# Optimization experiments

Hardware: AMD Instinct MI355X
Metric: run time of the kernel (lower is better)

Reference implementation:

```python
import jax, jax.numpy as jnp
import numpy as np

DIM = 512
HEADS = 8
P = 4  # split_size
SCALE = (DIM // HEADS) ** -0.5  # scale uses full dim//heads as in source


def conv1x1(x, w):
    # x: [b,c,h,w], w: [out,in]
    return jnp.einsum('oc,bchw->bohw', w, x)


def to_windows(t, p1, p2, h):
    # 'b (h d) (x p1) (y p2) -> (b x y) h (p1 p2) d'
    b, c, X, Y = t.shape
    d = c // h
    nx, ny = X // p1, Y // p2
    t = t.reshape(b, h, d, nx, p1, ny, p2)
    t = t.transpose(0, 3, 5, 1, 4, 6, 2)  # b nx ny h p1 p2 d
    return t.reshape(b * nx * ny, h, p1 * p2, d)


def from_windows(t, b, nx, ny, h, p1, p2, d):
    # '(b x y) h (p1 p2) d -> b (h d) (x p1) (y p2)'
    t = t.reshape(b, nx, ny, h, p1, p2, d)
    t = t.transpose(0, 3, 6, 1, 4, 2, 5)  # b h d nx p1 ny p2
    return t.reshape(b, h * d, nx * p1, ny * p2)


def setup_inputs() -> dict:
    key = jax.random.key(0)
    ks = jax.random.split(key, 6)
    s = 0.02
    return {
        'fmap': jax.random.normal(ks[0], (8, DIM, 64, 64), jnp.float32),
        'w_qk': jax.random.normal(ks[1], (2 * DIM, DIM), jnp.float32) * s,
        'w_v': jax.random.normal(ks[2], (DIM, DIM), jnp.float32) * s,
        'w_v_vert': jax.random.normal(ks[3], (DIM // 2, DIM // 2), jnp.float32) * s,
        'w_v_horiz': jax.random.normal(ks[4], (DIM // 2, DIM // 2), jnp.float32) * s,
        'w_proj': jax.random.normal(ks[5], (DIM, DIM), jnp.float32) * s,
    }


def reference(fmap, w_qk, w_v, w_v_vert, w_v_horiz, w_proj):
    b, c, X, Y = fmap.shape
    h, half = HEADS, c // 2
    d = half // h  # per-window head dim

    qk = conv1x1(fmap, w_qk)
    q, k = jnp.split(qk, 2, axis=1)
    v = conv1x1(fmap, w_v)

    # horizontal branch: first half channels, windows (X, P)
    qh = to_windows(q[:, :half], X, P, h)
    kh = to_windows(k[:, :half], X, P, h)
    vh = to_windows(v[:, :half], X, P, h)
    lepe_h = vh  # source bug: to_v_horizontal output discarded, raw v used as LePE

    # vertical branch: second half channels, windows (P, Y)
    qv = to_windows(q[:, half:], P, Y, h)
    kv = to_windows(k[:, half:], P, Y, h)
    vv = to_windows(v[:, half:], P, Y, h)
    lepe_v = to_windows(conv1x1(v[:, half:], w_v_vert), P, Y, h)

    def attend(qw, kw, vw, lepe):
        attn = jax.nn.softmax((qw * SCALE) @ jnp.swapaxes(kw, -1, -2), axis=-1)
        return attn @ vw + lepe

    out_h = attend(qh, kh, vh, lepe_h)
    out_v = attend(qv, kv, vv, lepe_v)

    oh = from_windows(out_h, b, X // X, Y // P, h, X, P, d)
    ov = from_windows(out_v, b, X // P, Y // Y, h, P, Y, d)
    out = jnp.concatenate([oh, ov], axis=1)
    return fmap + conv1x1(out, w_proj)
```

## Files before the change

kernel.cpp:

```cpp
#include <hip/hip_runtime.h>
#include <hip/hip_bf16.h>

#define NPIX 4096
#define SCALE_L2E 0.18033688f

typedef unsigned short ushort_t;
typedef __attribute__((ext_vector_type(8))) short bf16x8;
typedef __attribute__((ext_vector_type(4))) float f32x4;
typedef __attribute__((ext_vector_type(8))) unsigned short us8;

__device__ __forceinline__ float bf2f(ushort_t u) {
  union { unsigned int i; float f; } v; v.i = ((unsigned int)u) << 16; return v.f;
}
__device__ __forceinline__ ushort_t f2bf(float f) {
  union { float f; unsigned int i; } v; v.f = f;
  unsigned int r = v.i + 0x7fffu + ((v.i >> 16) & 1u);
  return (ushort_t)(r >> 16);
}
__device__ __forceinline__ unsigned int cvtpk(float lo, float hi) {
  unsigned int r;
  asm volatile("v_cvt_pk_bf16_f32 %0, %1, %2" : "=v"(r) : "v"(lo), "v"(hi));
  return r;
}

__device__ __forceinline__ void gload16(const void* g, void* l) {
  __builtin_amdgcn_global_load_lds(
      (const __attribute__((address_space(1))) void*)g,
      (__attribute__((address_space(3))) void*)l, 16, 0, 0);
}

#define VMW(N) asm volatile("s_waitcnt vmcnt(" #N ")" ::: "memory")
#define BARRS do { __builtin_amdgcn_s_barrier(); \
                   __builtin_amdgcn_sched_barrier(0); } while (0)

__global__ __launch_bounds__(256) void prep_w(const float* __restrict__ wqk,
                                              const float* __restrict__ wv,
                                              const float* __restrict__ wproj,
                                              ushort_t* __restrict__ WQKV,
                                              ushort_t* __restrict__ WPb) {
  const int i = (blockIdx.x * 256 + threadIdx.x) * 4;
  const int seg = i >> 18, off = i & 262143;
  const float* src;
  ushort_t* dst;
  float sc = 1.0f;
  if (seg == 0)      { src = wqk;          dst = WQKV;               sc = SCALE_L2E; }
  else if (seg == 1) { src = wqk + 262144; dst = WQKV + 262144; }
  else if (seg == 2) { src = wv;           dst = WQKV + 2 * 262144; }
  else               { src = wproj;        dst = WPb; }
  const float4 v = *(const float4*)&src[off];
  ushort4 o = make_ushort4(f2bf(v.x * sc), f2bf(v.y * sc),
                           f2bf(v.z * sc), f2bf(v.w * sc));
  *(ushort4*)&dst[off] = o;
}

__global__ __launch_bounds__(256) void lepe_w(const float* __restrict__ wvv,
                                              const float* __restrict__ wv,
                                              ushort_t* __restrict__ out) {
  const int i = blockIdx.x, tid = threadIdx.x;
  float a0 = 0.f, a1 = 0.f;
  for (int c = 0; c < 256; ++c) {
    const float wc = wvv[i * 256 + c];
    a0 = fmaf(wc, wv[(size_t)(256 + c) * 512 + tid], a0);
    a1 = fmaf(wc, wv[(size_t)(256 + c) * 512 + 256 + tid], a1);
  }
  out[(size_t)i * 512 + tid] = f2bf(a0);
  out[(size_t)i * 512 + 256 + tid] = f2bf(a1);
}

__global__ __launch_bounds__(256) void transpose_cast(const float* __restrict__ fmap,
                                                      ushort_t* __restrict__ XT) {
  const int b = blockIdx.z, p0 = blockIdx.x * 64, c0 = blockIdx.y * 64;
  const int tid = threadIdx.x;
  __shared__ float t[64][65];
  const float* src = fmap + ((size_t)b * 512 + c0) * NPIX + p0;
  const int pr = tid & 63;
  #pragma unroll
  for (int i = 0; i < 16; ++i) {
    const int cr = i * 4 + (tid >> 6);
    t[cr][pr] = src[(size_t)cr * NPIX + pr];
  }
  __syncthreads();
  const int pw = tid >> 2, cwb = (tid & 3) * 16;
  us8 o0, o1;
  #pragma unroll
  for (int i = 0; i < 8; ++i) o0[i] = f2bf(t[cwb + i][pw]);
  #pragma unroll
  for (int i = 0; i < 8; ++i) o1[i] = f2bf(t[cwb + 8 + i][pw]);
  ushort_t* dst = XT + ((size_t)b * NPIX + p0 + pw) * 512 + c0 + cwb;
  *(us8*)&dst[0] = o0;
  *(us8*)&dst[8] = o1;
}

__global__ __launch_bounds__(256) void gemm128(
    const ushort_t* __restrict__ A, const ushort_t* __restrict__ B,
    ushort_t* __restrict__ qkT, ushort_t* __restrict__ vbuf,
    float* __restrict__ outF, const float* __restrict__ Res, int mode)
{
  const int b = blockIdx.z;
  const int p0 = blockIdx.x * 128;
  const int o0 = blockIdx.y * 128;
  const int tid = threadIdx.x;
  const int lane = tid & 63, w = tid >> 6;
  const int wrow = (w >> 1) * 64, wcol = (w & 1) * 64;
  const int g = lane >> 4, q16 = lane & 15;

  __shared__ __attribute__((aligned(16))) ushort_t lds[3 * 8192];

  const ushort_t* Bb = B + (size_t)b * NPIX * 512;

  f32x4 acc[4][4];
  #pragma unroll
  for (int m = 0; m < 4; ++m)
    #pragma unroll
    for (int n = 0; n < 4; ++n) acc[m][n] = (f32x4){0.f, 0.f, 0.f, 0.f};

  auto Ap = [&](int buf) { return lds + buf * 8192; };
  auto Bp = [&](int buf) { return lds + buf * 8192 + 4096; };

  auto stage = [&](int buf, int kb) {
    #pragma unroll
    for (int i = 0; i < 2; ++i) {
      const int r = w * 32 + i * 16 + (lane >> 2);
      const int cs = (lane & 3) ^ ((r >> 1) & 3);
      gload16(&A[(size_t)(o0 + r) * 512 + kb + cs * 8], Ap(buf) + (w * 32 + i * 16) * 32);
      gload16(&Bb[(size_t)(p0 + r) * 512 + kb + cs * 8], Bp(buf) + (w * 32 + i * 16) * 32);
    }
  };

  stage(0, 0);
  stage(1, 32);
  VMW(4);
  BARRS;

  #pragma unroll
  for (int kt = 0; kt < 16; ++kt) {
    const int c = kt % 3;
    if (kt < 14) stage((kt + 2) % 3, (kt + 2) * 32);
    bf16x8 af[4], bfr[4];
    #pragma unroll
    for (int m = 0; m < 4; ++m) {
      const int rr = wrow + m * 16 + q16;
      af[m] = *(const bf16x8*)&Ap(c)[rr * 32 + (g ^ ((rr >> 1) & 3)) * 8];
    }
    #pragma unroll
    for (int n = 0; n < 4; ++n) {
      const int rr = wcol + n * 16 + q16;
      bfr[n] = *(const bf16x8*)&Bp(c)[rr * 32 + (g ^ ((rr >> 1) & 3)) * 8];
    }
    __builtin_amdgcn_s_setprio(1);
    #pragma unroll
    for (int m = 0; m < 4; ++m)
      #pragma unroll
      for (int n = 0; n < 4; ++n)
        acc[m][n] = __builtin_amdgcn_mfma_f32_16x16x32_bf16(af[m], bfr[n], acc[m][n], 0, 0, 0);
    __builtin_amdgcn_s_setprio(0);
    if (kt < 14) { VMW(4); BARRS; }
    else if (kt == 14) { VMW(0); BARRS; }
  }

  const int fr = lane & 15, fq = lane >> 4;
  if (mode == 0) {
    if (o0 < 1024) {
      ushort_t* CT = qkT + (size_t)b * NPIX * 1024;
      #pragma unroll
      for (int m = 0; m < 4; ++m)
        #pragma unroll
        for (int n = 0; n < 4; ++n) {
          const int pix = p0 + wcol + n * 16 + fr;
          const int chb = o0 + wrow + m * 16 + fq * 4;
          ushort4 s4 = make_ushort4(f2bf(acc[m][n][0]), f2bf(acc[m][n][1]),
                                    f2bf(acc[m][n][2]), f2bf(acc[m][n][3]));
          *(ushort4*)&CT[(size_t)pix * 1024 + chb] = s4;
        }
    } else {
      ushort_t* C = vbuf + (size_t)b * 768 * NPIX;
      #pragma unroll
      for (int m = 0; m < 4; ++m)
        #pragma unroll
        for (int n = 0; n < 4; ++n) {
          const int col = p0 + wcol + n * 16 + fr;
          #pragma unroll
          for (int j = 0; j < 4; ++j) {
            const int row = o0 - 1024 + wrow + m * 16 + fq * 4 + j;
            C[(size_t)row * NPIX + col] = f2bf(acc[m][n][j]);
          }
        }
    }
  } else {
    float* C = outF + (size_t)b * 512 * NPIX;
    const float* R = Res + (size_t)b * 512 * NPIX;
    #pragma unroll
    for (int m = 0; m < 4; ++m)
      #pragma unroll
      for (int n = 0; n < 4; ++n) {
        const int col = p0 + wcol + n * 16 + fr;
        #pragma unroll
        for (int j = 0; j < 4; ++j) {
          const int row = o0 + wrow + m * 16 + fq * 4 + j;
          const size_t idx = (size_t)row * NPIX + col;
          C[idx] = acc[m][n][j] + R[idx];
        }
      }
  }
}

__global__ __launch_bounds__(256) void attn_mfma(const ushort_t* __restrict__ qkT,
                                                 const ushort_t* __restrict__ vbuf,
                                                 ushort_t* __restrict__ attT) {
  const int hh = blockIdx.x, wi = blockIdx.y, vert = blockIdx.z;
  const int b = wi >> 4, iw = wi & 15;
  const int tid = threadIdx.x;
  const int lane = tid & 63, w = tid >> 6;
  const int g = lane >> 4, q16 = lane & 15;
  const int qbase = w * 64;

  __shared__ __attribute__((aligned(16))) ushort_t K_lds[256 * 32];
  __shared__ __attribute__((aligned(16))) ushort_t VT_lds[32 * 256];
  __shared__ __attribute__((aligned(16))) ushort_t P_lds[4][64 * 40];

  const ushort_t* QKb = qkT + (size_t)b * NPIX * 1024;

  #pragma unroll
  for (int it = 0; it < 4; ++it) {
    const int j = w * 64 + it * 16 + (lane >> 2);
    const int cs = (lane & 3) ^ ((j >> 1) & 3);
    const int pj = vert ? iw * 256 + j : (j >> 2) * 64 + iw * 4 + (j & 3);
    gload16(&QKb[(size_t)pj * 1024 + 512 + hh * 32 + cs * 8],
            &K_lds[(w * 64 + it * 16) * 32]);
  }
  const ushort_t* Vg = vbuf + ((size_t)b * 768 + vert * 256 + hh * 32) * (size_t)NPIX;
  #pragma unroll
  for (int it = 0; it < 8; ++it) {
    const int d = it * 4 + w;
    const int jg = lane;
    const int pb = vert ? iw * 256 + jg * 4 : jg * 64 + iw * 4;
    const ushort4 v4 = *(const ushort4*)&Vg[(size_t)d * NPIX + pb];
    *(ushort4*)&VT_lds[d * 256 + (((jg >> 1) ^ d) << 3) + ((jg & 1) << 2)] = v4;
  }
  bf16x8 qf[4];
  #pragma unroll
  for (int qt = 0; qt < 4; ++qt) {
    const int q = qbase + qt * 16 + q16;
    const int qp = vert ? iw * 256 + q : (q >> 2) * 64 + iw * 4 + (q & 3);
    qf[qt] = *(const bf16x8*)&QKb[(size_t)qp * 1024 + hh * 32 + g * 8];
  }
  __syncthreads();

  float l[4] = {0.f, 0.f, 0.f, 0.f};
  f32x4 o[4][2];
  #pragma unroll
  for (int qt = 0; qt < 4; ++qt) {
    o[qt][0] = (f32x4){0.f, 0.f, 0.f, 0.f};
    o[qt][1] = (f32x4){0.f, 0.f, 0.f, 0.f};
  }

  const f32x4 zero4 = (f32x4){0.f, 0.f, 0.f, 0.f};
  const int kc = g ^ ((q16 >> 1) & 3);

  for (int jc = 0; jc < 8; ++jc) {
    bf16x8 kf0 = *(const bf16x8*)&K_lds[(jc * 32 + q16) * 32 + kc * 8];
    bf16x8 kf1 = *(const bf16x8*)&K_lds[(jc * 32 + 16 + q16) * 32 + kc * 8];
    f32x4 st[2][4];
    #pragma unroll
    for (int qt = 0; qt < 4; ++qt) {
      st[0][qt] = __builtin_amdgcn_mfma_f32_16x16x32_bf16(kf0, qf[qt], zero4, 0, 0, 0);
      st[1][qt] = __builtin_amdgcn_mfma_f32_16x16x32_bf16(kf1, qf[qt], zero4, 0, 0, 0);
    }
    #pragma unroll
    for (int qt = 0; qt < 4; ++qt) {
      const float p00 = exp2f(st[0][qt][0]), p01 = exp2f(st[0][qt][1]);
      const float p02 = exp2f(st[0][qt][2]), p03 = exp2f(st[0][qt][3]);
      const float p10 = exp2f(st[1][qt][0]), p11 = exp2f(st[1][qt][1]);
      const float p12 = exp2f(st[1][qt][2]), p13 = exp2f(st[1][qt][3]);
      float rs = ((p00 + p01) + (p02 + p03)) + ((p10 + p11) + (p12 + p13));
      rs += __shfl_xor(rs, 16);
      rs += __shfl_xor(rs, 32);
      l[qt] += rs;
      uint2 pk0, pk1;
      pk0.x = cvtpk(p00, p01); pk0.y = cvtpk(p02, p03);
      pk1.x = cvtpk(p10, p11); pk1.y = cvtpk(p12, p13);
      *(uint2*)&P_lds[w][(qt * 16 + q16) * 40 + g * 4]      = pk0;
      *(uint2*)&P_lds[w][(qt * 16 + q16) * 40 + 16 + g * 4] = pk1;
    }
    const int vc0 = (jc * 4 + g) ^ q16;
    const int vc1 = (jc * 4 + g) ^ (16 + q16);
    bf16x8 vf0 = *(const bf16x8*)&VT_lds[q16 * 256 + vc0 * 8];
    bf16x8 vf1 = *(const bf16x8*)&VT_lds[(16 + q16) * 256 + vc1 * 8];
    #pragma unroll
    for (int qt = 0; qt < 4; ++qt) {
      bf16x8 pf = *(const bf16x8*)&P_lds[w][(qt * 16 + q16) * 40 + g * 8];
      o[qt][0] = __builtin_amdgcn_mfma_f32_16x16x32_bf16(pf, vf0, o[qt][0], 0, 0, 0);
      o[qt][1] = __builtin_amdgcn_mfma_f32_16x16x32_bf16(pf, vf1, o[qt][1], 0, 0, 0);
    }
  }

  const int ch = vert * 256 + hh * 32;
  const ushort_t* Lg = vbuf + ((size_t)b * 768 + 512 + hh * 32) * (size_t)NPIX;
  #pragma unroll
  for (int qt = 0; qt < 4; ++qt) {
    const float linv = 1.f / l[qt];
    float li[4];
    #pragma unroll
    for (int jj = 0; jj < 4; ++jj) li[jj] = __shfl(linv, g * 4 + jj);
    #pragma unroll
    for (int dt = 0; dt < 2; ++dt) {
      const int d = dt * 16 + q16;
      #pragma unroll
      for (int jj = 0; jj < 4; ++jj) {
        const int q = qbase + qt * 16 + g * 4 + jj;
        float lep;
        if (vert) lep = bf2f(Lg[(size_t)d * NPIX + iw * 256 + q]);
        else      lep = bf2f(VT_lds[d * 256 + (((q >> 3) ^ d) << 3) + (q & 7)]);
        const int pix = vert ? iw * 256 + q : (q >> 2) * 64 + iw * 4 + (q & 3);
        attT[((size_t)b * NPIX + pix) * 512 + ch + d] = f2bf(o[qt][dt][jj] * li[jj] + lep);
      }
    }
  }
}

extern "C" void kernel_launch(void* const* d_in, const int* in_sizes, int n_in,
                              void* d_out, int out_size, void* d_ws, size_t ws_size,
                              hipStream_t stream) {
  const float* fmap     = (const float*)d_in[0];
  const float* w_qk     = (const float*)d_in[1];
  const float* w_v      = (const float*)d_in[2];
  const float* w_v_vert = (const float*)d_in[3];
  const float* w_proj   = (const float*)d_in[5];
  float* out = (float*)d_out;

  ushort_t* XT   = (ushort_t*)d_ws;
  ushort_t* qkT  = XT + (size_t)8 * NPIX * 512;
  ushort_t* vbuf = qkT + (size_t)8 * NPIX * 1024;
  ushort_t* attT = vbuf + (size_t)8 * 768 * NPIX;
  ushort_t* WQKV = attT + (size_t)8 * NPIX * 512;
  ushort_t* WPb  = WQKV + (size_t)1792 * 512;

  dim3 blk(256);
  prep_w<<<1024, blk, 0, stream>>>(w_qk, w_v, w_proj, WQKV, WPb);
  lepe_w<<<256, blk, 0, stream>>>(w_v_vert, w_v, WQKV + (size_t)1536 * 512);
  transpose_cast<<<dim3(64, 8, 8), blk, 0, stream>>>(fmap, XT);
  gemm128<<<dim3(32, 14, 8), blk, 0, stream>>>(
      WQKV, XT, qkT, vbuf, nullptr, nullptr, 0);
  attn_mfma<<<dim3(8, 128, 2), blk, 0, stream>>>(qkT, vbuf, attT);
  gemm128<<<dim3(32, 4, 8), blk, 0, stream>>>(
      WPb, attT, nullptr, nullptr, out, fmap, 1);
}
```

Measured before the change: 225.4 us.

## Fuse fmap transpose and bf16 cast into QKV GEMM B-tile loading

Removes the separate transpose_cast kernel and its XT workspace. The QKV GEMM now reads fp32 fmap directly through registers, converts it to bf16 with v_cvt_pk_bf16_f32, and writes swizzled tiles into LDS, with the global loads for tile k+2 issued before the MFMAs and committed afterwards. This saves one kernel launch and a bf16 write/read of the activations. In exchange, the 14 output-channel blocks each re-read fp32 fmap, which is twice the bytes of the old bf16 copy. The register-path B loads also add VGPR pressure and lgkm waits in the main loop.

```diff
diff --git a/kernel.cpp b/kernel.cpp
--- a/kernel.cpp
+++ b/kernel.cpp
@@ -30,6 +30,7 @@
 }
 
 #define VMW(N) asm volatile("s_waitcnt vmcnt(" #N ")" ::: "memory")
+#define LGKMW  asm volatile("s_waitcnt lgkmcnt(0)" ::: "memory")
 #define BARRS do { __builtin_amdgcn_s_barrier(); \
                    __builtin_amdgcn_sched_barrier(0); } while (0)
 
@@ -67,34 +68,9 @@
   out[(size_t)i * 512 + 256 + tid] = f2bf(a1);
 }
 
-__global__ __launch_bounds__(256) void transpose_cast(const float* __restrict__ fmap,
-                                                      ushort_t* __restrict__ XT) {
-  const int b = blockIdx.z, p0 = blockIdx.x * 64, c0 = blockIdx.y * 64;
-  const int tid = threadIdx.x;
-  __shared__ float t[64][65];
-  const float* src = fmap + ((size_t)b * 512 + c0) * NPIX + p0;
-  const int pr = tid & 63;
-  #pragma unroll
-  for (int i = 0; i < 16; ++i) {
-    const int cr = i * 4 + (tid >> 6);
-    t[cr][pr] = src[(size_t)cr * NPIX + pr];
-  }
-  __syncthreads();
-  const int pw = tid >> 2, cwb = (tid & 3) * 16;
-  us8 o0, o1;
-  #pragma unroll
-  for (int i = 0; i < 8; ++i) o0[i] = f2bf(t[cwb + i][pw]);
-  #pragma unroll
-  for (int i = 0; i < 8; ++i) o1[i] = f2bf(t[cwb + 8 + i][pw]);
-  ushort_t* dst = XT + ((size_t)b * NPIX + p0 + pw) * 512 + c0 + cwb;
-  *(us8*)&dst[0] = o0;
-  *(us8*)&dst[8] = o1;
-}
-
-__global__ __launch_bounds__(256) void gemm128(
-    const ushort_t* __restrict__ A, const ushort_t* __restrict__ B,
-    ushort_t* __restrict__ qkT, ushort_t* __restrict__ vbuf,
-    float* __restrict__ outF, const float* __restrict__ Res, int mode)
+__global__ __launch_bounds__(256) void gemm_qkv(
+    const ushort_t* __restrict__ A, const float* __restrict__ fmap,
+    ushort_t* __restrict__ qkT, ushort_t* __restrict__ vbuf)
 {
   const int b = blockIdx.z;
   const int p0 = blockIdx.x * 128;
@@ -106,6 +82,135 @@
 
   __shared__ __attribute__((aligned(16))) ushort_t lds[3 * 8192];
 
+  const float* Bf = fmap + (size_t)b * 512 * NPIX;
+
+  f32x4 acc[4][4];
+  #pragma unroll
+  for (int m = 0; m < 4; ++m)
+    #pragma unroll
+    for (int n = 0; n < 4; ++n) acc[m][n] = (f32x4){0.f, 0.f, 0.f, 0.f};
+
+  auto Ap = [&](int buf) { return lds + buf * 8192; };
+  auto Bp = [&](int buf) { return lds + buf * 8192 + 4096; };
+
+  float breg[2][8];
+  auto loadBf = [&](int kb) {
+    #pragma unroll
+    for (int i = 0; i < 2; ++i) {
+      const int idx = i * 256 + tid;
+      const int r = idx & 127;
+      const int cc = idx >> 7;
+      const float* src = Bf + (size_t)(kb + cc * 8) * NPIX + p0 + r;
+      #pragma unroll
+      for (int j = 0; j < 8; ++j)
+        breg[i][j] = src[(size_t)j * NPIX];
+    }
+  };
+  auto commitB = [&](int buf) {
+    #pragma unroll
+    for (int i = 0; i < 2; ++i) {
+      const int idx = i * 256 + tid;
+      const int r = idx & 127;
+      const int cc = idx >> 7;
+      uint4 pk;
+      pk.x = cvtpk(breg[i][0], breg[i][1]);
+      pk.y = cvtpk(breg[i][2], breg[i][3]);
+      pk.z = cvtpk(breg[i][4], breg[i][5]);
+      pk.w = cvtpk(breg[i][6], breg[i][7]);
+      *(uint4*)&Bp(buf)[r * 32 + ((cc ^ ((r >> 1) & 3)) << 3)] = pk;
+    }
+  };
+  auto stageA = [&](int buf, int kb) {
+    #pragma unroll
+    for (int i = 0; i < 2; ++i) {
+      const int rr = w * 32 + i * 16 + (lane >> 2);
+      const int cs = (lane & 3) ^ ((rr >> 1) & 3);
+      gload16(&A[(size_t)(o0 + rr) * 512 + kb + cs * 8],
+              Ap(buf) + (w * 32 + i * 16) * 32);
+    }
+  };
+
+  loadBf(0);  stageA(0, 0);  commitB(0);
+  loadBf(32); stageA(1, 32); commitB(1);
+  LGKMW; VMW(2);
+  BARRS;
+
+  #pragma unroll
+  for (int kt = 0; kt < 16; ++kt) {
+    const int c = kt % 3;
+    if (kt < 14) {
+      loadBf((kt + 2) * 32);
+      stageA((kt + 2) % 3, (kt + 2) * 32);
+    }
+    bf16x8 af[4], bfr[4];
+    #pragma unroll
+    for (int m = 0; m < 4; ++m) {
+      const int rr = wrow + m * 16 + q16;
+      af[m] = *(const bf16x8*)&Ap(c)[rr * 32 + (g ^ ((rr >> 1) & 3)) * 8];
+    }
+    #pragma unroll
+    for (int n = 0; n < 4; ++n) {
+      const int rr = wcol + n * 16 + q16;
+      bfr[n] = *(const bf16x8*)&Bp(c)[rr * 32 + (g ^ ((rr >> 1) & 3)) * 8];
+    }
+    __builtin_amdgcn_s_setprio(1);
+    #pragma unroll
+    for (int m = 0; m < 4; ++m)
+      #pragma unroll
+      for (int n = 0; n < 4; ++n)
+        acc[m][n] = __builtin_amdgcn_mfma_f32_16x16x32_bf16(af[m], bfr[n], acc[m][n], 0, 0, 0);
+    __builtin_amdgcn_s_setprio(0);
+    if (kt < 14) {
+      commitB((kt + 2) % 3);
+      LGKMW; VMW(2); BARRS;
+    } else if (kt == 14) {
+      LGKMW; VMW(0); BARRS;
+    }
+  }
+
+  const int fr = lane & 15, fq = lane >> 4;
+  if (o0 < 1024) {
+    ushort_t* CT = qkT + (size_t)b * NPIX * 1024;
+    #pragma unroll
+    for (int m = 0; m < 4; ++m)
+      #pragma unroll
+      for (int n = 0; n < 4; ++n) {
+        const int pix = p0 + wcol + n * 16 + fr;
+        const int chb = o0 + wrow + m * 16 + fq * 4;
+        ushort4 s4 = make_ushort4(f2bf(acc[m][n][0]), f2bf(acc[m][n][1]),
+                                  f2bf(acc[m][n][2]), f2bf(acc[m][n][3]));
+        *(ushort4*)&CT[(size_t)pix * 1024 + chb] = s4;
+      }
+  } else {
+    ushort_t* C = vbuf + (size_t)b * 768 * NPIX;
+    #pragma unroll
+    for (int m = 0; m < 4; ++m)
+      #pragma unroll
+      for (int n = 0; n < 4; ++n) {
+        const int col = p0 + wcol + n * 16 + fr;
+        #pragma unroll
+        for (int j = 0; j < 4; ++j) {
+          const int row = o0 - 1024 + wrow + m * 16 + fq * 4 + j;
+          C[(size_t)row * NPIX + col] = f2bf(acc[m][n][j]);
+        }
+      }
+  }
+}
+
+__global__ __launch_bounds__(256) void gemm_proj(
+    const ushort_t* __restrict__ A, const ushort_t* __restrict__ B,
+    float* __restrict__ outF, const float* __restrict__ Res)
+{
+  const int b = blockIdx.z;
+  const int p0 = blockIdx.x * 128;
+  const int o0 = blockIdx.y * 128;
+  const int tid = threadIdx.x;
+  const int lane = tid & 63, w = tid >> 6;
+  const int wrow = (w >> 1) * 64, wcol = (w & 1) * 64;
+  const int g = lane >> 4, q16 = lane & 15;
+
+  __shared__ __attribute__((aligned(16))) ushort_t lds[3 * 8192];
+
   const ushort_t* Bb = B + (size_t)b * NPIX * 512;
 
   f32x4 acc[4][4];
@@ -159,49 +264,20 @@
   }
 
   const int fr = lane & 15, fq = lane >> 4;
-  if (mode == 0) {
-    if (o0 < 1024) {
-      ushort_t* CT = qkT + (size_t)b * NPIX * 1024;
-      #pragma unroll
-      for (int m = 0; m < 4; ++m)
-        #pragma unroll
-        for (int n = 0; n < 4; ++n) {
-          const int pix = p0 + wcol + n * 16 + fr;
-          const int chb = o0 + wrow + m * 16 + fq * 4;
-          ushort4 s4 = make_ushort4(f2bf(acc[m][n][0]), f2bf(acc[m][n][1]),
-                                    f2bf(acc[m][n][2]), f2bf(acc[m][n][3]));
-          *(ushort4*)&CT[(size_t)pix * 1024 + chb] = s4;
-        }
-    } else {
-      ushort_t* C = vbuf + (size_t)b * 768 * NPIX;
-      #pragma unroll
-      for (int m = 0; m < 4; ++m)
-        #pragma unroll
-        for (int n = 0; n < 4; ++n) {
-          const int col = p0 + wcol + n * 16 + fr;
-          #pragma unroll
-          for (int j = 0; j < 4; ++j) {
-            const int row = o0 - 1024 + wrow + m * 16 + fq * 4 + j;
-            C[(size_t)row * NPIX + col] = f2bf(acc[m][n][j]);
-          }
-        }
-    }
-  } else {
-    float* C = outF + (size_t)b * 512 * NPIX;
-    const float* R = Res + (size_t)b * 512 * NPIX;
-    #pragma unroll
-    for (int m = 0; m < 4; ++m)
-      #pragma unroll
-      for (int n = 0; n < 4; ++n) {
-        const int col = p0 + wcol + n * 16 + fr;
-        #pragma unroll
-        for (int j = 0; j < 4; ++j) {
-          const int row = o0 + wrow + m * 16 + fq * 4 + j;
-          const size_t idx = (size_t)row * NPIX + col;
-          C[idx] = acc[m][n][j] + R[idx];
-        }
+  float* C = outF + (size_t)b * 512 * NPIX;
+  const float* R = Res + (size_t)b * 512 * NPIX;
+  #pragma unroll
+  for (int m = 0; m < 4; ++m)
+    #pragma unroll
+    for (int n = 0; n < 4; ++n) {
+      const int col = p0 + wcol + n * 16 + fr;
+      #pragma unroll
+      for (int j = 0; j < 4; ++j) {
+        const int row = o0 + wrow + m * 16 + fq * 4 + j;
+        const size_t idx = (size_t)row * NPIX + col;
+        C[idx] = acc[m][n][j] + R[idx];
       }
-  }
+    }
 }
 
 __global__ __launch_bounds__(256) void attn_mfma(const ushort_t* __restrict__ qkT,
@@ -328,8 +404,7 @@
   const float* w_proj   = (const float*)d_in[5];
   float* out = (float*)d_out;
 
-  ushort_t* XT   = (ushort_t*)d_ws;
-  ushort_t* qkT  = XT + (size_t)8 * NPIX * 512;
+  ushort_t* qkT  = (ushort_t*)d_ws;
   ushort_t* vbuf = qkT + (size_t)8 * NPIX * 1024;
   ushort_t* attT = vbuf + (size_t)8 * 768 * NPIX;
   ushort_t* WQKV = attT + (size_t)8 * NPIX * 512;
@@ -338,10 +413,7 @@
   dim3 blk(256);
   prep_w<<<1024, blk, 0, stream>>>(w_qk, w_v, w_proj, WQKV, WPb);
   lepe_w<<<256, blk, 0, stream>>>(w_v_vert, w_v, WQKV + (size_t)1536 * 512);
-  transpose_cast<<<dim3(64, 8, 8), blk, 0, stream>>>(fmap, XT);
-  gemm128<<<dim3(32, 14, 8), blk, 0, stream>>>(
-      WQKV, XT, qkT, vbuf, nullptr, nullptr, 0);
+  gemm_qkv<<<dim3(32, 14, 8), blk, 0, stream>>>(WQKV, fmap, qkT, vbuf);
   attn_mfma<<<dim3(8, 128, 2), blk, 0, stream>>>(qkT, vbuf, attT);
-  gemm128<<<dim3(32, 4, 8), blk, 0, stream>>>(
-      WPb, attT, nullptr, nullptr, out, fmap, 1);
-}
+  gemm_proj<<<dim3(32, 4, 8), blk, 0, stream>>>(WPb, attT, out, fmap);
+}
```

Result: no change. 223.8 us (-0.7%).
